# Kernel tuning notes

Measured on AMD Instinct MI355X. Metric: run time of the kernel, lower is better.

Reference implementation:

```python
import jax, jax.numpy as jnp
import numpy as np

B, S, HID = 2, 2048, 4096
H, P, N, G, K = 128, 64, 128, 8, 4      # heads, head_dim, ssm_state, groups, conv kernel
INTER = H * P                           # 8192
CONV_DIM = INTER + 2 * G * N            # 10240
CHUNK = 128
EPS = 1e-5
DT_MIN, DT_MAX = 0.0, 100.0


def setup_inputs() -> dict:
    key = jax.random.key(0)
    ks = jax.random.split(key, 4)
    proj = INTER + CONV_DIM + H
    return {
        "x": jax.random.normal(ks[0], (B, S, HID), jnp.float32),
        "in_proj_w": jax.random.normal(ks[1], (proj, HID), jnp.float32) * 0.02,
        "conv_w": jax.random.normal(ks[2], (CONV_DIM, 1, K), jnp.float32) * 0.2,
        "conv_b": jnp.zeros((CONV_DIM,), jnp.float32),
        "dt_bias": jnp.ones((H,), jnp.float32),
        "A_log": jnp.log(jnp.arange(1, H + 1, dtype=jnp.float32)),
        "D": jnp.ones((H,), jnp.float32),
        "norm_w": jnp.ones((INTER,), jnp.float32),
        "out_proj_w": jax.random.normal(ks[3], (HID, INTER), jnp.float32) * 0.02,
    }


def _segsum(a):
    # a: (..., c) -> (..., c, c); [i, j] = sum_{k=j+1..i} a[k] for i >= j, else -inf
    c = a.shape[-1]
    s = jnp.cumsum(a, axis=-1)
    diff = s[..., :, None] - s[..., None, :]
    mask = jnp.tril(jnp.ones((c, c), dtype=bool))
    return jnp.where(mask, diff, -jnp.inf)


def reference(x, in_proj_w, conv_w, conv_b, dt_bias, A_log, D, norm_w, out_proj_w):
    b, s, _ = x.shape
    proj = jnp.einsum('bsd,ed->bse', x, in_proj_w)
    gate = proj[..., :INTER]
    hBC = proj[..., INTER:INTER + CONV_DIM]
    dt = proj[..., INTER + CONV_DIM:]                       # (b, s, H)

    # depthwise causal conv1d + silu
    xc = jnp.transpose(hBC, (0, 2, 1))                      # (b, conv_dim, s)
    xc = jax.lax.conv_general_dilated(xc, conv_w, (1,), [(K - 1, 0)],
                                      dimension_numbers=('NCH', 'OIH', 'NCH'),
                                      feature_group_count=CONV_DIM)
    xc = xc + conv_b[None, :, None]
    hBC = jax.nn.silu(jnp.transpose(xc, (0, 2, 1)))

    hs = hBC[..., :INTER].reshape(b, s, H, P)
    Bm = hBC[..., INTER:INTER + G * N].reshape(b, s, G, N)
    Cm = hBC[..., INTER + G * N:].reshape(b, s, G, N)

    A = -jnp.exp(A_log)                                     # (H,)
    dt = jnp.clip(jax.nn.softplus(dt + dt_bias), DT_MIN, DT_MAX)

    rep = H // G
    Bh = jnp.repeat(Bm, rep, axis=2)                        # (b, s, H, N)
    Ch = jnp.repeat(Cm, rep, axis=2)

    nc = s // CHUNK
    xch = (hs * dt[..., None]).reshape(b, nc, CHUNK, H, P)  # dt-scaled input, chunked
    Bc = Bh.reshape(b, nc, CHUNK, H, N)
    Cc = Ch.reshape(b, nc, CHUNK, H, N)
    A_dt = (dt * A).reshape(b, nc, CHUNK, H).transpose(0, 3, 1, 2)  # (b, H, nc, c)
    A_cum = jnp.cumsum(A_dt, axis=-1)

    # intra-chunk (diagonal) contribution
    L = jnp.exp(_segsum(A_dt))                              # (b, H, nc, c, c)
    Y_diag = jnp.einsum('bzlhn,bzshn,bhzls,bzshp->bzlhp', Cc, Bc, L, xch)

    # per-chunk final states
    decay_states = jnp.exp(A_cum[..., -1:] - A_cum)         # (b, H, nc, c)
    states = jnp.einsum('bzlhn,bhzl,bzlhp->bzhpn', Bc, decay_states, xch)

    # inter-chunk recurrence (initial state = 0)
    states_p = jnp.concatenate([jnp.zeros_like(states[:, :1]), states], axis=1)  # (b, nc+1, H, P, N)
    A_last = jnp.pad(A_cum[..., -1], ((0, 0), (0, 0), (1, 0)))                   # (b, H, nc+1)
    decay_chunk = jnp.exp(_segsum(A_last))                                        # (b, H, nc+1, nc+1)
    new_states = jnp.einsum('bhzc,bchpn->bzhpn', decay_chunk, states_p)
    prev = new_states[:, :-1]                                # state entering each chunk

    Y_off = jnp.einsum('bzlhn,bzhpn,bhzl->bzlhp', Cc, prev, jnp.exp(A_cum))
    Y = (Y_diag + Y_off).reshape(b, s, H, P) + hs * D[None, None, :, None]
    y = Y.reshape(b, s, INTER)

    # gated grouped RMSNorm (norm_before_gate=False)
    g = y * jax.nn.silu(gate)
    gg = g.reshape(b, s, G, INTER // G)
    var = jnp.mean(gg * gg, axis=-1, keepdims=True)
    gg = gg * jax.lax.rsqrt(var + EPS)
    out = gg.reshape(b, s, INTER) * norm_w

    return jnp.einsum('bsi,oi->bso', out, out_proj_w)
```

## Files before the change

### kernel.cpp

```cpp
#include <hip/hip_runtime.h>
#include <hip/hip_bf16.h>
#include <cstdint>
#include <cstddef>

#define DEVI __device__ __forceinline__

#define BB 2
#define S_LEN 2048
#define HID_DIM 4096
#define NH 128
#define PD 64
#define NS 128
#define NG 8
#define INTER 8192
#define CONVD 10240
#define PROJ 18560
#define PROJP 18688
#define NC 16
#define BS 4096
#define GN 1024

using short8 = __attribute__((ext_vector_type(8))) short;
using short4v = __attribute__((ext_vector_type(4))) short;
using f32x4  = __attribute__((ext_vector_type(4))) float;
using bf16x8 = __attribute__((ext_vector_type(8))) __bf16;

DEVI float bf2f(short u) {
  union { unsigned int i; float f; } v;
  v.i = ((unsigned int)(unsigned short)u) << 16;
  return v.f;
}
DEVI short f2bf(float f) {
  union { float ff; unsigned int i; } v; v.ff = f;
  unsigned int x = v.i;
  return (short)((x + 0x7fffu + ((x >> 16) & 1u)) >> 16);
}
DEVI f32x4 mfma16(short8 a, short8 b, f32x4 c) {
  return __builtin_amdgcn_mfma_f32_16x16x32_bf16(
      __builtin_bit_cast(bf16x8, a), __builtin_bit_cast(bf16x8, b), c, 0, 0, 0);
}
DEVI void gl_lds16(const short* g, short* l) {
  __builtin_amdgcn_global_load_lds(
      (const __attribute__((address_space(1))) void*)g,
      (__attribute__((address_space(3))) void*)l, 16, 0, 0);
}
DEVI float sigmoidf_(float x) { return 1.f / (1.f + __expf(-x)); }

__global__ __launch_bounds__(256) void cvt_f32_bf16_k(const float* __restrict__ in,
                                                      short* __restrict__ out, size_t n) {
  size_t i = ((size_t)blockIdx.x * 256 + threadIdx.x) * 8;
  if (i + 8 > n) return;
  float4 a = *(const float4*)(in + i);
  float4 b = *(const float4*)(in + i + 4);
  short8 o;
  o[0] = f2bf(a.x); o[1] = f2bf(a.y); o[2] = f2bf(a.z); o[3] = f2bf(a.w);
  o[4] = f2bf(b.x); o[5] = f2bf(b.y); o[6] = f2bf(b.z); o[7] = f2bf(b.w);
  *(short8*)(out + i) = o;
}


#define STG(ISB, BUF, KH, TILE) do { \
  const short* _src = (ISB) ? Bt : A; \
  const int _r0 = (ISB) ? n0 : m0; \
  short* _lb = lds_ + ((ISB) ? 32768 : 0) + ((BUF)*2+(KH))*8192; \
  const int _kt = (TILE)*64 + (KH)*32; \
  { int _row = (wid*2)*16 + srow; int _sl = sps ^ ((_row>>1)&3); \
    gl_lds16(_src + (size_t)(_r0+_row)*K + _kt + _sl*8, _lb + (wid*2)*512); } \
  { int _row = (wid*2+1)*16 + srow; int _sl = sps ^ ((_row>>1)&3); \
    gl_lds16(_src + (size_t)(_r0+_row)*K + _kt + _sl*8, _lb + (wid*2+1)*512); } \
} while(0)

#define VM4 asm volatile("s_waitcnt vmcnt(4)" ::: "memory")
#define VM0 asm volatile("s_waitcnt vmcnt(0)" ::: "memory")

#define LDAF(DST, BUF, KH, MIH) do { \
  _Pragma("unroll") \
  for (int _m = 0; _m < 4; ++_m) { \
    int _row = wr*128 + ((MIH)*4+_m)*16 + fr; \
    DST[_m] = *(const short8*)(lds_ + ((BUF)*2+(KH))*8192 + _row*32 + ((slot ^ ((_row>>1)&3))<<3)); \
  } \
} while(0)

#define LDBF(DST, BUF, KH) do { \
  _Pragma("unroll") \
  for (int _n = 0; _n < 4; ++_n) { \
    int _row = wc*64 + _n*16 + fr; \
    DST[_n] = *(const short8*)(lds_ + 32768 + ((BUF)*2+(KH))*8192 + _row*32 + ((slot ^ ((_row>>1)&3))<<3)); \
  } \
} while(0)

#define MFMA16X(MIH, AF, BF) do { \
  _Pragma("unroll") \
  for (int _m = 0; _m < 4; ++_m) \
    _Pragma("unroll") \
    for (int _n = 0; _n < 4; ++_n) \
      acc[(MIH)*4+_m][_n] = mfma16(AF[_m], BF[_n], acc[(MIH)*4+_m][_n]); \
} while(0)

#define ITER(CB, NB, TNEXT, DOSTG, VMW) do { \
  if (DOSTG) { STG(0, NB, 0, TNEXT); STG(1, NB, 0, TNEXT); } \
  VMW; \
  __builtin_amdgcn_s_barrier(); \
  LDAF(af0, CB, 0, 0); LDAF(af1, CB, 1, 0); \
  LDBF(bf0, CB, 0); LDBF(bf1, CB, 1); \
  __builtin_amdgcn_s_setprio(1); \
  MFMA16X(0, af0, bf0); \
  MFMA16X(0, af1, bf1); \
  __builtin_amdgcn_s_setprio(0); \
  if (DOSTG) { STG(0, NB, 1, TNEXT); STG(1, NB, 1, TNEXT); } \
  LDAF(af0, CB, 0, 1); LDAF(af1, CB, 1, 1); \
  __builtin_amdgcn_s_setprio(1); \
  MFMA16X(1, af0, bf0); \
  MFMA16X(1, af1, bf1); \
  __builtin_amdgcn_s_setprio(0); \
  asm volatile("s_waitcnt lgkmcnt(0)" ::: "memory"); \
  __builtin_amdgcn_s_barrier(); \
} while(0)

template<int CB16>
__global__ __launch_bounds__(512, 2) void gemm256_k(const short* __restrict__ A,
                                                    const short* __restrict__ Bt,
                                                    void* __restrict__ Cout,
                                                    int Nstride, int K, int ntn) {
  __shared__ short lds_[65536];
  const int tid = threadIdx.x, wid = tid >> 6, lane = tid & 63;
  const int nwg = gridDim.x, orig = blockIdx.x;
  const int swz = (orig & 7) * (nwg >> 3) + (orig >> 3);
  const int per_group = ntn << 3;
  const int group = swz / per_group;
  const int rem = swz - group * per_group;
  const int m0 = (group * 8 + (rem & 7)) * 256;
  const int n0 = (rem >> 3) * 256;
  const int wr = wid >> 2, wc = wid & 3;
  const int fr = lane & 15, slot = lane >> 4;
  const int srow = lane >> 2, sps = lane & 3;

  f32x4 acc[8][4] = {};
  short8 af0[4], af1[4], bf0[4], bf1[4];
  const int NT = K >> 6;

  STG(0, 0, 0, 0); STG(1, 0, 0, 0); STG(0, 0, 1, 0); STG(1, 0, 1, 0);

  for (int ii = 0; ii < (NT >> 1) - 1; ++ii) {
    const int t = 2 * ii;
    ITER(0, 1, t + 1, 1, VM4);
    ITER(1, 0, t + 2, 1, VM4);
  }
  ITER(0, 1, NT - 1, 1, VM4);
  ITER(1, 0, 0, 0, VM0);

  const int er = (lane >> 4) * 4, ec = lane & 15;
  if (CB16) {
    short* C = (short*)Cout;
#pragma unroll
    for (int mi = 0; mi < 8; ++mi)
#pragma unroll
      for (int j = 0; j < 4; ++j) {
        size_t base = (size_t)(m0 + wr * 128 + mi * 16 + er + j) * Nstride + n0 + wc * 64 + ec;
#pragma unroll
        for (int ni = 0; ni < 4; ++ni) C[base + ni * 16] = f2bf(acc[mi][ni][j]);
      }
  } else {
    float* C = (float*)Cout;
#pragma unroll
    for (int mi = 0; mi < 8; ++mi)
#pragma unroll
      for (int j = 0; j < 4; ++j) {
        size_t base = (size_t)(m0 + wr * 128 + mi * 16 + er + j) * Nstride + n0 + wc * 64 + ec;
#pragma unroll
        for (int ni = 0; ni < 4; ++ni) C[base + ni * 16] = acc[mi][ni][j];
      }
  }
}

__global__ __launch_bounds__(256) void conv_silu_k(const short* __restrict__ projb,
                                                   const float* __restrict__ convw,
                                                   const float* __restrict__ convb,
                                                   short* __restrict__ hbc) {
  const int c = blockIdx.x * 256 + threadIdx.x;
  const int s0 = blockIdx.y * 256;
  const int b = blockIdx.z;
  const size_t rb = (size_t)b * S_LEN;
  const float* wp = convw + (size_t)c * 4;
  const float w0 = wp[0], w1 = wp[1], w2 = wp[2], w3 = wp[3];
  const float bias = convb[c];
  const short* pcol = projb + INTER + c;
  float x1 = 0.f, x2 = 0.f, x3 = 0.f;
  if (s0 > 0) {
    x3 = bf2f(pcol[(rb + s0 - 3) * PROJP]);
    x2 = bf2f(pcol[(rb + s0 - 2) * PROJP]);
    x1 = bf2f(pcol[(rb + s0 - 1) * PROJP]);
  }
  for (int s = s0; s < s0 + 256; ++s) {
    float v = bf2f(pcol[(rb + s) * PROJP]);
    float acc = bias + w0 * x3 + w1 * x2 + w2 * x1 + w3 * v;
    float o = acc * sigmoidf_(acc);
    hbc[(rb + s) * CONVD + c] = f2bf(o);
    x3 = x2; x2 = x1; x1 = v;
  }
}

__global__ __launch_bounds__(128) void acum_k(const short* __restrict__ projb,
                                              const float* __restrict__ dt_bias,
                                              const float* __restrict__ A_log,
                                              float* __restrict__ dtT,
                                              float* __restrict__ acum) {
  const int l = threadIdx.x;
  const int lane = l & 63, wv = l >> 6;
  const int z = blockIdx.x, h = blockIdx.y, b = blockIdx.z;
  const float A = -__expf(A_log[h]);
  __shared__ float w0tot;
  const int r = b * S_LEN + z * 128 + l;
  float xv = bf2f(projb[(size_t)r * PROJP + INTER + CONVD + h]) + dt_bias[h];
  float sp = (xv > 20.f) ? xv : log1pf(__expf(xv));
  sp = fminf(fmaxf(sp, 0.f), 100.f);
  const size_t base = ((size_t)(b * NH + h)) * S_LEN + z * 128;
  dtT[base + l] = sp;
  float val = sp * A;
#pragma unroll
  for (int off = 1; off < 64; off <<= 1) {
    float t = __shfl_up(val, off, 64);
    if (lane >= off) val += t;
  }
  if (wv == 0 && lane == 63) w0tot = val;
  __syncthreads();
  if (wv == 1) val += w0tot;
  acum[base + l] = val;
}

__global__ __launch_bounds__(512) void states_k(const short* __restrict__ hbc,
                                                const float* __restrict__ dtT,
                                                const float* __restrict__ acum,
                                                float* __restrict__ states) {
  __shared__ short sBT[128 * 136];
  __shared__ short sxdt2[2][64 * 136];
  const int tid = threadIdx.x, wid = tid >> 6, lane = tid & 63;
  const int g = blockIdx.x, z = blockIdx.y, b = blockIdx.z;
  const size_t srow0 = (size_t)(b * S_LEN + z * 128);
  const short* hrow = hbc + srow0 * CONVD;

  {
    const int l = tid & 127, n0b = (tid >> 7) * 32;
    const short* src = hrow + (size_t)l * CONVD + INTER + g * NS + n0b;
    short8 v0 = *(const short8*)(src);
    short8 v1 = *(const short8*)(src + 8);
    short8 v2 = *(const short8*)(src + 16);
    short8 v3 = *(const short8*)(src + 24);
#pragma unroll
    for (int j = 0; j < 8; ++j) {
      sBT[(n0b + j) * 136 + l] = v0[j];
      sBT[(n0b + 8 + j) * 136 + l] = v1[j];
      sBT[(n0b + 16 + j) * 136 + l] = v2[j];
      sBT[(n0b + 24 + j) * 136 + l] = v3[j];
    }
  }

  const int fr = lane & 15, fk8 = (lane >> 4) * 8;
  const int er = (lane >> 4) * 4, ec = lane & 15;
  const int pband = (wid & 3) * 16, nhalf = (wid >> 2) * 64;
  const int s2 = tid & 63, p0w = (tid >> 6) * 8;

  float cdv0, cdv1; short8 cr0, cr1;
  {
    const int h = g * 16;
    const float* acg = acum + ((size_t)(b * NH + h)) * S_LEN + z * 128;
    const float* dts = dtT + ((size_t)(b * NH + h)) * S_LEN + z * 128;
    const float acL = acg[127];
    cdv0 = dts[2 * s2] * __expf(acL - acg[2 * s2]);
    cdv1 = dts[2 * s2 + 1] * __expf(acL - acg[2 * s2 + 1]);
    const short* rsrc = hrow + (size_t)(2 * s2) * CONVD + (size_t)h * PD + p0w;
    cr0 = *(const short8*)(rsrc);
    cr1 = *(const short8*)(rsrc + CONVD);
  }
  {
    unsigned int* x32 = (unsigned int*)sxdt2[0];
#pragma unroll
    for (int j = 0; j < 8; ++j) {
      unsigned int lo = (unsigned short)f2bf(bf2f(cr0[j]) * cdv0);
      unsigned int hi = (unsigned short)f2bf(bf2f(cr1[j]) * cdv1);
      x32[(p0w + j) * 68 + s2] = lo | (hi << 16);
    }
  }
  __syncthreads();

  for (int hh = 0; hh < 16; ++hh) {
    const int h = g * 16 + hh;
    float ndv0 = 0.f, ndv1 = 0.f; short8 nr0, nr1;
    if (hh < 15) {
      const int h2 = h + 1;
      const float* acg = acum + ((size_t)(b * NH + h2)) * S_LEN + z * 128;
      const float* dts = dtT + ((size_t)(b * NH + h2)) * S_LEN + z * 128;
      const float acL = acg[127];
      ndv0 = dts[2 * s2] * __expf(acL - acg[2 * s2]);
      ndv1 = dts[2 * s2 + 1] * __expf(acL - acg[2 * s2 + 1]);
      const short* rsrc = hrow + (size_t)(2 * s2) * CONVD + (size_t)h2 * PD + p0w;
      nr0 = *(const short8*)(rsrc);
      nr1 = *(const short8*)(rsrc + CONVD);
    }
    const short* sx = sxdt2[hh & 1];
    f32x4 st[4] = {};
#pragma unroll
    for (int kk = 0; kk < 4; ++kk) {
      short8 a = *(const short8*)(sx + (pband + fr) * 136 + kk * 32 + fk8);
#pragma unroll
      for (int ni = 0; ni < 4; ++ni) {
        short8 bb = *(const short8*)(sBT + (nhalf + ni * 16 + fr) * 136 + kk * 32 + fk8);
        st[ni] = mfma16(a, bb, st[ni]);
      }
    }
    float* stp = states + (((size_t)(b * NC + z)) * NH + h) * (size_t)(NS * PD);
#pragma unroll
    for (int ni = 0; ni < 4; ++ni)
#pragma unroll
      for (int j = 0; j < 4; ++j)
        stp[(pband + er + j) * NS + nhalf + ni * 16 + ec] = st[ni][j];
    if (hh < 15) {
      unsigned int* x32 = (unsigned int*)sxdt2[(hh + 1) & 1];
#pragma unroll
      for (int j = 0; j < 8; ++j) {
        unsigned int lo = (unsigned short)f2bf(bf2f(nr0[j]) * ndv0);
        unsigned int hi = (unsigned short)f2bf(bf2f(nr1[j]) * ndv1);
        x32[(p0w + j) * 68 + s2] = lo | (hi << 16);
      }
    }
    __syncthreads();
  }
}

__global__ __launch_bounds__(256) void scan_k(float* __restrict__ states,
                                              const float* __restrict__ acum) {
  const int h = blockIdx.x, b = blockIdx.y;
  const int tid = threadIdx.x;
  float* stp = states + ((size_t)(b * NC * NH) + h) * (size_t)(NS * PD);
  const size_t cst = (size_t)NH * NS * PD;
  const float* ac = acum + ((size_t)(b * NH + h)) * S_LEN;
  float E[32];
#pragma unroll
  for (int i = 0; i < 32; ++i) E[i] = 0.f;
  const int n = tid & 127, pg = tid >> 7;
  for (int zz = 0; zz < NC; ++zz) {
    float* sz = stp + (size_t)zz * cst;
    short* pvb = (short*)sz;
    float tmp[32];
#pragma unroll
    for (int i = 0; i < 32; ++i) tmp[i] = sz[i * 256 + tid];
    __syncthreads();
    float dec = __expf(ac[zz * 128 + 127]);
#pragma unroll
    for (int i = 0; i < 32; ++i) {
      int p = i * 2 + pg;
      pvb[p * 128 + n] = f2bf(E[i]);
      E[i] = dec * E[i] + tmp[i];
    }
    __syncthreads();
  }
}

#define RDSW(BUF, ROWBASE, KK) \
  (*(const short8*)((BUF) + ((ROWBASE) + fr) * 128 + ((((KK) * 4 + slot4) ^ sw7) << 3)))

#define WRX(DST, D0, D1, R0, R1) do { \
  unsigned int* _x = (unsigned int*)(DST); \
  _Pragma("unroll") \
  for (int _j = 0; _j < 8; ++_j) { \
    unsigned int _lo = (unsigned short)f2bf(bf2f(R0[_j]) * (D0)); \
    unsigned int _hi = (unsigned short)f2bf(bf2f(R1[_j]) * (D1)); \
    _x[(p0w + _j) * 64 + ((((s2 >> 2) ^ _j) << 2) | (s2 & 3))] = _lo | (_hi << 16); \
  } \
} while (0)

#define WRP(DST, P0, P1) do { \
  int _p = tid >> 3; int _s0 = (tid & 7) * 2; int _m = _p & 7; \
  *(short8*)((DST) + _p * 128 + ((_s0 ^ _m) << 3)) = P0; \
  *(short8*)((DST) + _p * 128 + (((_s0 + 1) ^ _m) << 3)) = P1; \
} while (0)

#define LOADH_Y(H, DT0, DT1, ACS, ACL, R0, R1, P0, P1) do { \
  const float* _ac = acum + ((size_t)(b * NH + (H))) * S_LEN + z * 128; \
  const float* _dts = dtT + ((size_t)(b * NH + (H))) * S_LEN + z * 128; \
  DT0 = _dts[2 * s2]; DT1 = _dts[2 * s2 + 1]; \
  _Pragma("unroll") \
  for (int _si = 0; _si < 8; ++_si) ACS[_si] = _ac[_si * 16 + ec]; \
  _Pragma("unroll") \
  for (int _j = 0; _j < 4; ++_j) ACL[_j] = _ac[lrow + er + _j]; \
  const short* _rs = hrow + (size_t)(2 * s2) * CONVD + (size_t)(H) * PD + p0w; \
  R0 = *(const short8*)(_rs); R1 = *(const short8*)(_rs + CONVD); \
  const short* _pv = (const short*)(states + (((size_t)(b * NC + z)) * NH + (H)) * (size_t)(NS * PD)); \
  P0 = *(const short8*)(_pv + tid * 16); P1 = *(const short8*)(_pv + tid * 16 + 8); \
} while (0)

__global__ __launch_bounds__(512) void yfull_k(const short* __restrict__ hbc,
                                               const short* __restrict__ projb,
                                               const float* __restrict__ dtT,
                                               const float* __restrict__ acum,
                                               const float* __restrict__ states,
                                               const float* __restrict__ Dv,
                                               const float* __restrict__ norm_w,
                                               short* __restrict__ normed) {
  __shared__ short lds[66560];
  __shared__ float sScale[128];
  __shared__ float sNW[1024];
  short* sC = lds;
  short* sB = lds + 16384;
  short* sx0 = lds + 32768;
  short* sp0 = lds + 40960;
  const int tid = threadIdx.x, wid = tid >> 6, lane = tid & 63;
  short* sPw = lds + 49152 + wid * 2176;
  const int g = blockIdx.x, z = blockIdx.y, b = blockIdx.z;
  const size_t srow0 = (size_t)(b * S_LEN + z * 128);
  const short* hrow = hbc + srow0 * CONVD;

  {
    const int slot_g = (lane & 15) ^ (((wid & 1) << 2) | (lane >> 4));
    const int n0_ = slot_g * 8;
#pragma unroll
    for (int it = 0; it < 4; ++it) {
      int s = it * 32 + wid * 4 + (lane >> 4);
      gl_lds16(hrow + (size_t)s * CONVD + INTER + GN + g * NS + n0_, sC + (it * 32 + wid * 4) * 128);
      gl_lds16(hrow + (size_t)s * CONVD + INTER + g * NS + n0_, sB + (it * 32 + wid * 4) * 128);
    }
  }
  for (int i = tid; i < 1024; i += 512) sNW[i] = norm_w[g * 1024 + i];
  __syncthreads();

  const int fr = lane & 15, fk8 = (lane >> 4) * 8;
  const int slot4 = lane >> 4, sw7 = lane & 7;
  const int er = (lane >> 4) * 4, ec = lane & 15;
  const int lrow = wid * 16;
  const int s2 = tid & 63, p0w = (tid >> 6) * 8;

  float cdt0, cdt1, cacS[8], cacl[4];
  short8 cr0, cr1, cp0, cp1;
  LOADH_Y(g * 16, cdt0, cdt1, cacS, cacl, cr0, cr1, cp0, cp1);

  f32x4 sc[8] = {};
#pragma unroll
  for (int kk = 0; kk < 4; ++kk) {
    short8 a = RDSW(sC, lrow, kk);
#pragma unroll
    for (int si = 0; si < 8; ++si) {
      short8 bv = RDSW(sB, si * 16, kk);
      sc[si] = mfma16(a, bv, sc[si]);
    }
  }
  WRX(sx0, cdt0, cdt1, cr0, cr1);
  WRP(sp0, cp0, cp1);
  __syncthreads();

  float rssq[4] = {0.f, 0.f, 0.f, 0.f};

  for (int hh = 0; hh < 16; ++hh) {
    const int h = g * 16 + hh;
    float ndt0 = 0.f, ndt1 = 0.f, nacS[8], nacl[4];
    short8 nr0, nr1, np0, np1;
    if (hh < 15) LOADH_Y(h + 1, ndt0, ndt1, nacS, nacl, nr0, nr1, np0, np1);

    short* sx = (hh & 1) ? sB : sx0;
    short* sp = (hh & 1) ? (sB + 8192) : sp0;

#pragma unroll
    for (int j = 0; j < 4; ++j) {
      int lloc = er + j;
      float acl = cacl[j];
#pragma unroll
      for (int si = 0; si < 8; ++si) {
        int sI = si * 16 + ec;
        float v = (sI <= lrow + lloc) ? sc[si][j] * __expf(acl - cacS[si]) : 0.f;
        sPw[lloc * 136 + sI] = f2bf(v);
      }
    }
    f32x4 yd[4] = {}, yo[4] = {};
#pragma unroll
    for (int kk = 0; kk < 4; ++kk) {
      short8 ap = *(const short8*)(sPw + fr * 136 + kk * 32 + fk8);
      short8 acf = RDSW(sC, lrow, kk);
#pragma unroll
      for (int ni = 0; ni < 4; ++ni) {
        short8 bv = RDSW(sx, ni * 16, kk);
        yd[ni] = mfma16(ap, bv, yd[ni]);
        short8 bp = RDSW(sp, ni * 16, kk);
        yo[ni] = mfma16(acf, bp, yo[ni]);
      }
    }
    const float Dh = Dv[h];
#pragma unroll
    for (int j = 0; j < 4; ++j) {
      int l = lrow + er + j;
      float e_ac = __expf(cacl[j]);
#pragma unroll
      for (int ni = 0; ni < 4; ++ni) {
        int p = ni * 16 + ec;
        float hs = bf2f(hrow[(size_t)l * CONVD + (size_t)h * PD + p]);
        float y = yd[ni][j] + yo[ni][j] * e_ac + hs * Dh;
        float gate = bf2f(projb[(srow0 + l) * (size_t)PROJP + (size_t)h * PD + p]);
        float gg = y * gate * sigmoidf_(gate);
        normed[(srow0 + l) * (size_t)INTER + (size_t)h * PD + p] = f2bf(gg);
        rssq[j] += gg * gg;
      }
    }
    if (hh < 15) {
      short* nx = (hh & 1) ? sx0 : sB;
      short* npv = (hh & 1) ? sp0 : (sB + 8192);
      WRX(nx, ndt0, ndt1, nr0, nr1);
      WRP(npv, np0, np1);
      cdt0 = ndt0; cdt1 = ndt1; cr0 = nr0; cr1 = nr1; cp0 = np0; cp1 = np1;
#pragma unroll
      for (int si = 0; si < 8; ++si) cacS[si] = nacS[si];
#pragma unroll
      for (int j = 0; j < 4; ++j) cacl[j] = nacl[j];
    }
    __syncthreads();
  }

#pragma unroll
  for (int j = 0; j < 4; ++j) {
#pragma unroll
    for (int m = 1; m <= 8; m <<= 1) rssq[j] += __shfl_xor(rssq[j], m, 64);
  }
  if (ec == 0) {
#pragma unroll
    for (int j = 0; j < 4; ++j) sScale[lrow + er + j] = rsqrtf(rssq[j] * (1.f / 1024.f) + 1e-5f);
  }
  __syncthreads();

  for (int e = tid * 8; e < 128 * 1024; e += 4096) {
    int row = e >> 10, ch = e & 1023;
    short* gp = normed + (srow0 + row) * (size_t)INTER + g * 1024 + ch;
    short8 gv = *(const short8*)(gp);
    float scl = sScale[row];
    short8 o;
#pragma unroll
    for (int q = 0; q < 8; ++q) o[q] = f2bf(bf2f(gv[q]) * scl * sNW[ch + q]);
    *(short8*)(gp) = o;
  }
}

extern "C" void kernel_launch(void* const* d_in, const int* in_sizes, int n_in,
                              void* d_out, int out_size, void* d_ws, size_t ws_size,
                              hipStream_t stream) {
  const float* x     = (const float*)d_in[0];
  const float* w1    = (const float*)d_in[1];
  const float* convw = (const float*)d_in[2];
  const float* convb = (const float*)d_in[3];
  const float* dtb   = (const float*)d_in[4];
  const float* alog  = (const float*)d_in[5];
  const float* Dv    = (const float*)d_in[6];
  const float* nw    = (const float*)d_in[7];
  const float* w2    = (const float*)d_in[8];
  float* out = (float*)d_out;

  char* ws = (char*)d_ws;
  size_t off = 0;
  float* dtT = (float*)(ws + off);  off += (size_t)BB * NH * S_LEN * 4;
  float* acum = (float*)(ws + off); off += (size_t)BB * NH * S_LEN * 4;
  short* xb = (short*)(ws + off);   off += (size_t)BS * HID_DIM * 2;
  char* w1region = ws + off;        off += (size_t)PROJP * HID_DIM * 2;
  short* w1b = (short*)w1region;
  short* normed = (short*)w1region;
  short* w2b = (short*)(w1region + (size_t)BS * INTER * 2);
  short* projb = (short*)(ws + off); off += (size_t)BS * PROJP * 2;
  short* hbc = (short*)(ws + off);   off += (size_t)BS * CONVD * 2;
  float* states = (float*)(ws + off); off += (size_t)BB * NC * NH * NS * PD * 4;

  const size_t nx = (size_t)BS * HID_DIM;
  const size_t nw1 = (size_t)PROJ * HID_DIM;
  const size_t nw2 = (size_t)HID_DIM * INTER;

  cvt_f32_bf16_k<<<dim3(nx / 2048), 256, 0, stream>>>(x, xb, nx);
  cvt_f32_bf16_k<<<dim3(nw1 / 2048), 256, 0, stream>>>(w1, w1b, nw1);

  gemm256_k<1><<<dim3(16 * 73), 512, 0, stream>>>(xb, w1b, projb, PROJP, HID_DIM, 73);

  cvt_f32_bf16_k<<<dim3(nw2 / 2048), 256, 0, stream>>>(w2, w2b, nw2);

  conv_silu_k<<<dim3(CONVD / 256, S_LEN / 256, BB), 256, 0, stream>>>(projb, convw, convb, hbc);
  acum_k<<<dim3(NC, NH, BB), 128, 0, stream>>>(projb, dtb, alog, dtT, acum);

  states_k<<<dim3(NG, NC, BB), 512, 0, stream>>>(hbc, dtT, acum, states);
  scan_k<<<dim3(NH, BB), 256, 0, stream>>>(states, acum);
  yfull_k<<<dim3(NG, NC, BB), 512, 0, stream>>>(hbc, projb, dtT, acum, states, Dv, nw, normed);

  gemm256_k<0><<<dim3(16 * 16), 512, 0, stream>>>(normed, w2b, out, HID_DIM, INTER, 16);
}
```

Measured before the change: 1.171 ms.

## Fuse fp32-to-bf16 weight conversion into GEMM B-operand staging

The GEMM now reads the fp32 weight matrices directly through registers, converts them to bf16 and writes them into the swizzled LDS layout, instead of running separate conversion kernels for both weight matrices beforehand. This removes two full passes over the weights (read fp32, write bf16, reread bf16) and two kernel launches. In exchange, each GEMM tile loads twice the bytes of B from global memory, across all M-tiles. It also adds register pressure and VALU conversion work inside the pipelined main loop. Rows past the valid range are clamped rather than padded.

```diff
diff --git a/kernel.cpp b/kernel.cpp
--- a/kernel.cpp
+++ b/kernel.cpp
@@ -58,20 +58,43 @@
   *(short8*)(out + i) = o;
 }
 
-
-#define STG(ISB, BUF, KH, TILE) do { \
-  const short* _src = (ISB) ? Bt : A; \
-  const int _r0 = (ISB) ? n0 : m0; \
-  short* _lb = lds_ + ((ISB) ? 32768 : 0) + ((BUF)*2+(KH))*8192; \
+#define STGA(BUF, KH, TILE) do { \
+  short* _lb = lds_ + ((BUF)*2+(KH))*8192; \
   const int _kt = (TILE)*64 + (KH)*32; \
   { int _row = (wid*2)*16 + srow; int _sl = sps ^ ((_row>>1)&3); \
-    gl_lds16(_src + (size_t)(_r0+_row)*K + _kt + _sl*8, _lb + (wid*2)*512); } \
+    gl_lds16(A + (size_t)(m0+_row)*K + _kt + _sl*8, _lb + (wid*2)*512); } \
   { int _row = (wid*2+1)*16 + srow; int _sl = sps ^ ((_row>>1)&3); \
-    gl_lds16(_src + (size_t)(_r0+_row)*K + _kt + _sl*8, _lb + (wid*2+1)*512); } \
+    gl_lds16(A + (size_t)(m0+_row)*K + _kt + _sl*8, _lb + (wid*2+1)*512); } \
 } while(0)
 
+#define VM8 asm volatile("s_waitcnt vmcnt(8)" ::: "memory")
 #define VM4 asm volatile("s_waitcnt vmcnt(4)" ::: "memory")
 #define VM0 asm volatile("s_waitcnt vmcnt(0)" ::: "memory")
+
+#define LDBGF(TILE) do { \
+  int _brow = n0 + wid*32 + (lane>>1); if (_brow >= Nrows) _brow = Nrows - 1; \
+  const float* _bp = Btf + (size_t)_brow * K + (TILE)*64 + (lane&1)*16; \
+  b8[0] = *(const float4*)(_bp);      b8[1] = *(const float4*)(_bp + 4); \
+  b8[2] = *(const float4*)(_bp + 8);  b8[3] = *(const float4*)(_bp + 12); \
+  b8[4] = *(const float4*)(_bp + 32); b8[5] = *(const float4*)(_bp + 36); \
+  b8[6] = *(const float4*)(_bp + 40); b8[7] = *(const float4*)(_bp + 44); \
+} while(0)
+
+#define CVWRB(BUF) do { \
+  const int _row = wid*32 + (lane>>1); \
+  const int _sw = (_row>>1)&3; \
+  const int _sgb = (lane&1)*2; \
+  _Pragma("unroll") \
+  for (int _h = 0; _h < 2; ++_h) \
+    _Pragma("unroll") \
+    for (int _s = 0; _s < 2; ++_s) { \
+      float4 _x = b8[_h*4 + _s*2], _y = b8[_h*4 + _s*2 + 1]; \
+      short8 _o; \
+      _o[0]=f2bf(_x.x); _o[1]=f2bf(_x.y); _o[2]=f2bf(_x.z); _o[3]=f2bf(_x.w); \
+      _o[4]=f2bf(_y.x); _o[5]=f2bf(_y.y); _o[6]=f2bf(_y.z); _o[7]=f2bf(_y.w); \
+      *(short8*)(lds_ + 32768 + ((BUF)*2+_h)*8192 + _row*32 + (((_sgb+_s) ^ _sw)<<3)) = _o; \
+    } \
+} while(0)
 
 #define LDAF(DST, BUF, KH, MIH) do { \
   _Pragma("unroll") \
@@ -97,31 +120,33 @@
       acc[(MIH)*4+_m][_n] = mfma16(AF[_m], BF[_n], acc[(MIH)*4+_m][_n]); \
 } while(0)
 
-#define ITER(CB, NB, TNEXT, DOSTG, VMW) do { \
-  if (DOSTG) { STG(0, NB, 0, TNEXT); STG(1, NB, 0, TNEXT); } \
-  VMW; \
+#define ITERF(CB, NB, TNEXT, DOSTG, VMBAR) do { \
+  if (DOSTG) LDBGF(TNEXT); \
+  VMBAR; \
   __builtin_amdgcn_s_barrier(); \
   LDAF(af0, CB, 0, 0); LDAF(af1, CB, 1, 0); \
   LDBF(bf0, CB, 0); LDBF(bf1, CB, 1); \
+  if (DOSTG) STGA(NB, 0, TNEXT); \
   __builtin_amdgcn_s_setprio(1); \
   MFMA16X(0, af0, bf0); \
   MFMA16X(0, af1, bf1); \
   __builtin_amdgcn_s_setprio(0); \
-  if (DOSTG) { STG(0, NB, 1, TNEXT); STG(1, NB, 1, TNEXT); } \
+  if (DOSTG) STGA(NB, 1, TNEXT); \
   LDAF(af0, CB, 0, 1); LDAF(af1, CB, 1, 1); \
   __builtin_amdgcn_s_setprio(1); \
   MFMA16X(1, af0, bf0); \
   MFMA16X(1, af1, bf1); \
   __builtin_amdgcn_s_setprio(0); \
+  if (DOSTG) { VM4; CVWRB(NB); } \
   asm volatile("s_waitcnt lgkmcnt(0)" ::: "memory"); \
   __builtin_amdgcn_s_barrier(); \
 } while(0)
 
 template<int CB16>
 __global__ __launch_bounds__(512, 2) void gemm256_k(const short* __restrict__ A,
-                                                    const short* __restrict__ Bt,
+                                                    const float* __restrict__ Btf,
                                                     void* __restrict__ Cout,
-                                                    int Nstride, int K, int ntn) {
+                                                    int Nstride, int K, int ntn, int Nrows) {
   __shared__ short lds_[65536];
   const int tid = threadIdx.x, wid = tid >> 6, lane = tid & 63;
   const int nwg = gridDim.x, orig = blockIdx.x;
@@ -137,17 +162,22 @@
 
   f32x4 acc[8][4] = {};
   short8 af0[4], af1[4], bf0[4], bf1[4];
+  float4 b8[8];
   const int NT = K >> 6;
 
-  STG(0, 0, 0, 0); STG(1, 0, 0, 0); STG(0, 0, 1, 0); STG(1, 0, 1, 0);
+  LDBGF(0);
+  STGA(0, 0, 0); STGA(0, 1, 0);
+  VM4;
+  CVWRB(0);
+  asm volatile("s_waitcnt lgkmcnt(0)" ::: "memory");
 
   for (int ii = 0; ii < (NT >> 1) - 1; ++ii) {
     const int t = 2 * ii;
-    ITER(0, 1, t + 1, 1, VM4);
-    ITER(1, 0, t + 2, 1, VM4);
-  }
-  ITER(0, 1, NT - 1, 1, VM4);
-  ITER(1, 0, 0, 0, VM0);
+    ITERF(0, 1, t + 1, 1, VM8);
+    ITERF(1, 0, t + 2, 1, VM8);
+  }
+  ITERF(0, 1, NT - 1, 1, VM8);
+  ITERF(1, 0, 0, 0, VM0);
 
   const int er = (lane >> 4) * 4, ec = lane & 15;
   if (CB16) {
@@ -554,24 +584,16 @@
   float* dtT = (float*)(ws + off);  off += (size_t)BB * NH * S_LEN * 4;
   float* acum = (float*)(ws + off); off += (size_t)BB * NH * S_LEN * 4;
   short* xb = (short*)(ws + off);   off += (size_t)BS * HID_DIM * 2;
-  char* w1region = ws + off;        off += (size_t)PROJP * HID_DIM * 2;
-  short* w1b = (short*)w1region;
-  short* normed = (short*)w1region;
-  short* w2b = (short*)(w1region + (size_t)BS * INTER * 2);
+  short* normed = (short*)(ws + off); off += (size_t)BS * INTER * 2;
   short* projb = (short*)(ws + off); off += (size_t)BS * PROJP * 2;
   short* hbc = (short*)(ws + off);   off += (size_t)BS * CONVD * 2;
   float* states = (float*)(ws + off); off += (size_t)BB * NC * NH * NS * PD * 4;
 
   const size_t nx = (size_t)BS * HID_DIM;
-  const size_t nw1 = (size_t)PROJ * HID_DIM;
-  const size_t nw2 = (size_t)HID_DIM * INTER;
 
   cvt_f32_bf16_k<<<dim3(nx / 2048), 256, 0, stream>>>(x, xb, nx);
-  cvt_f32_bf16_k<<<dim3(nw1 / 2048), 256, 0, stream>>>(w1, w1b, nw1);
-
-  gemm256_k<1><<<dim3(16 * 73), 512, 0, stream>>>(xb, w1b, projb, PROJP, HID_DIM, 73);
-
-  cvt_f32_bf16_k<<<dim3(nw2 / 2048), 256, 0, stream>>>(w2, w2b, nw2);
+
+  gemm256_k<1><<<dim3(16 * 73), 512, 0, stream>>>(xb, w1, projb, PROJP, HID_DIM, 73, PROJ);
 
   conv_silu_k<<<dim3(CONVD / 256, S_LEN / 256, BB), 256, 0, stream>>>(projb, convw, convb, hbc);
   acum_k<<<dim3(NC, NH, BB), 128, 0, stream>>>(projb, dtb, alog, dtT, acum);
@@ -580,5 +602,5 @@
   scan_k<<<dim3(NH, BB), 256, 0, stream>>>(states, acum);
   yfull_k<<<dim3(NG, NC, BB), 512, 0, stream>>>(hbc, projb, dtT, acum, states, Dv, nw, normed);
 
-  gemm256_k<0><<<dim3(16 * 16), 512, 0, stream>>>(normed, w2b, out, HID_DIM, INTER, 16);
-}
+  gemm256_k<0><<<dim3(16 * 16), 512, 0, stream>>>(normed, w2, out, HID_DIM, INTER, 16, HID_DIM);
+}
```

Measured after the change: 1.686 ms. +44.0%, slower.
